# Kernel optimization log

Hardware: AMD Instinct MI355X
Metric: run time of the kernel (lower is better)

The kernel has to match this reference:

```python
import jax, jax.numpy as jnp
import numpy as np
import math

HIDDEN = 2048
N_HEADS = 16
HEAD_DIM = HIDDEN // N_HEADS  # 128
ROPE_THETA = 10000.0


def _rope_cos_sin(seq_len, dim, theta, dtype):
    # Megatron RotaryEmbedding: freqs = pos \outer inv_freq; emb = cat(freqs, freqs)
    inv_freq = 1.0 / (theta ** (jnp.arange(0, dim, 2, dtype=jnp.float32) / dim))
    pos = jnp.arange(seq_len, dtype=jnp.float32)
    freqs = jnp.outer(pos, inv_freq)            # [S, dim/2]
    emb = jnp.concatenate([freqs, freqs], -1)   # [S, dim]
    return jnp.cos(emb).astype(dtype), jnp.sin(emb).astype(dtype)


def _rotate_half(x):
    half = x.shape[-1] // 2
    return jnp.concatenate([-x[..., half:], x[..., :half]], axis=-1)


def setup_inputs() -> dict:
    key = jax.random.key(0)
    k1, k2, k3 = jax.random.split(key, 3)
    B, S = 2, 2048
    hidden_states = jax.random.normal(k1, (B, S, HIDDEN), dtype=jnp.float32)
    # torch Linear weights are [out_features, in_features]
    w_qkv = jax.random.normal(k2, (3 * HIDDEN, HIDDEN), dtype=jnp.float32) * (1.0 / math.sqrt(HIDDEN))
    w_o = jax.random.normal(k3, (HIDDEN, HIDDEN), dtype=jnp.float32) * (1.0 / math.sqrt(HIDDEN))
    return {"hidden_states": hidden_states, "w_qkv": w_qkv, "w_o": w_o}


def reference(hidden_states, w_qkv, w_o):
    B, S, H = hidden_states.shape
    # fused QKV projection: [B,S,H] @ [H, 3H] -> view (.., n_heads, 3, head_dim)
    mixed = jnp.einsum('bsh,oh->bso', hidden_states, w_qkv)
    mixed = mixed.reshape(B, S, N_HEADS, 3, HEAD_DIM)
    q, k, v = mixed[..., 0, :], mixed[..., 1, :], mixed[..., 2, :]  # [B,S,Hn,D]

    # fused split + RoPE (full rotary dim = head_dim)
    cos, sin = _rope_cos_sin(S, HEAD_DIM, ROPE_THETA, hidden_states.dtype)
    cos = cos[None, :, None, :]  # [1,S,1,D]
    sin = sin[None, :, None, :]
    q = q * cos + _rotate_half(q) * sin
    k = k * cos + _rotate_half(k) * sin

    # causal scaled-dot-product attention (flash_attn_func equivalent math)
    scale = 1.0 / math.sqrt(HEAD_DIM)
    scores = jnp.einsum('bqhd,bkhd->bhqk', q, k) * scale  # [B,Hn,S,S]
    causal = jnp.tril(jnp.ones((S, S), dtype=bool))
    scores = jnp.where(causal[None, None], scores, jnp.finfo(scores.dtype).min)
    probs = jax.nn.softmax(scores, axis=-1)
    attn = jnp.einsum('bhqk,bkhd->bqhd', probs, v)  # [B,S,Hn,D]

    attn = attn.reshape(B, S, H)
    out = jnp.einsum('bsh,oh->bso', attn, w_o)
    return out
```

## Files before the change

kernel.cpp:

```cpp
#include <hip/hip_runtime.h>
#include <hip/hip_bf16.h>
#include <cstdint>
#include <cstddef>

#define S_DIM 2048
#define H_DIM 2048
#define NHEAD 16
#define HD_DIM 128
#define O3    6144
#define BS    4096
#define NBH   32

typedef short  s16x4  __attribute__((ext_vector_type(4)));
typedef short  s16x8  __attribute__((ext_vector_type(8)));
typedef __bf16 bf16x8 __attribute__((ext_vector_type(8)));
typedef float  f32x4  __attribute__((ext_vector_type(4)));

__device__ __forceinline__ unsigned short f2bf(float f) {
  unsigned int b = __float_as_uint(f);
  b += 0x7FFFu + ((b >> 16) & 1u);
  return (unsigned short)(b >> 16);
}
__device__ __forceinline__ float bf2f(unsigned short u) {
  return __uint_as_float(((unsigned int)u) << 16);
}
__device__ __forceinline__ bf16x8 load8(const unsigned short* p) {
  s16x8 r = *(const s16x8*)p;
  return __builtin_bit_cast(bf16x8, r);
}
__device__ __forceinline__ f32x4 mfma_bf16(bf16x8 a, bf16x8 b, f32x4 c) {
  return __builtin_amdgcn_mfma_f32_16x16x32_bf16(a, b, c, 0, 0, 0);
}
__device__ __forceinline__ void gload_lds16(const void* g, void* l) {
  __builtin_amdgcn_global_load_lds(
      (__attribute__((address_space(1))) unsigned int*)g,
      (__attribute__((address_space(3))) unsigned int*)l, 16, 0, 0);
}

__global__ void prep_kernel(const float* __restrict__ hid,
                            const float* __restrict__ wqkv,
                            const float* __restrict__ wo,
                            unsigned short* __restrict__ hid_b,
                            unsigned short* __restrict__ wqkv_b,
                            unsigned short* __restrict__ wo_b,
                            float* __restrict__ cosT,
                            float* __restrict__ sinT) {
  const int nA = 2097152, nB = 3145728, nC = 1048576, nD = 131072;
  const int total = nA + nB + nC + nD;
  int stride = gridDim.x * blockDim.x;
  for (int i = blockIdx.x * blockDim.x + threadIdx.x; i < total; i += stride) {
    if (i < nA + nB + nC) {
      const float* src; unsigned short* dst; int j;
      if (i < nA)            { src = hid;  dst = hid_b;  j = i; }
      else if (i < nA + nB)  { src = wqkv; dst = wqkv_b; j = i - nA; }
      else                   { src = wo;   dst = wo_b;   j = i - nA - nB; }
      float4 v = ((const float4*)src)[j];
      ushort4 o;
      o.x = f2bf(v.x); o.y = f2bf(v.y); o.z = f2bf(v.z); o.w = f2bf(v.w);
      ((ushort4*)dst)[j] = o;
    } else {
      int idx = i - nA - nB - nC;
      int s = idx >> 6, d = idx & 63;
      float inv = expf(-((float)d / 64.0f) * 9.210340371976184f);
      float ang = (float)s * inv;
      float sn, cs;
      sincosf(ang, &sn, &cs);
      cosT[idx] = cs;
      sinT[idx] = sn;
    }
  }
}

template <bool OUT_BF16, bool QKV_MAP>
__global__ __launch_bounds__(512, 1)
void gemm3b_kernel(const unsigned short* __restrict__ A,
                   const unsigned short* __restrict__ Bw,
                   void* __restrict__ C, int M, int N, int K) {
  __shared__ __align__(16) unsigned short lA[3][128 * 64];
  __shared__ __align__(16) unsigned short lB[3][256 * 64];
  const int tid  = threadIdx.x;
  const int wave = tid >> 6, lane = tid & 63;
  const int wm = wave >> 2, wn = wave & 3;
  const int lg = lane >> 4, ll = lane & 15;

  const int nbx = gridDim.x;
  const int id  = blockIdx.y * nbx + blockIdx.x;
  int m_tile, n_tile;
  if (QKV_MAP) {
    const int k = id & 7, q = id >> 3;
    const int ng = q >> 5, r = q & 31;
    m_tile = (k >> 1) * 8 + (r & 7);
    n_tile = (k & 1) * 12 + ng * 4 + (r >> 3);
  } else {
    const int nwg = gridDim.x * gridDim.y;
    const int swz = (id & 7) * (nwg >> 3) + (id >> 3);
    m_tile = swz / nbx;
    n_tile = swz % nbx;
  }
  const int m0 = m_tile * 128, n0 = n_tile * 256;

  f32x4 acc[4][4];
#pragma unroll
  for (int i = 0; i < 4; ++i)
#pragma unroll
    for (int j = 0; j < 4; ++j) acc[i][j] = (f32x4){0.f, 0.f, 0.f, 0.f};

  const unsigned short* aP[2];
  const unsigned short* bP[4];
  int aD[2], bD[4];
#pragma unroll
  for (int i = 0; i < 2; ++i) {
    int cb = (i * 8 + wave) * 64 + lane;
    int cs = cb ^ ((cb >> 3) & 7);
    aP[i] = A + (size_t)(m0 + (cs >> 3)) * K + (cs & 7) * 8;
    aD[i] = cb * 8;
  }
#pragma unroll
  for (int i = 0; i < 4; ++i) {
    int cb = (i * 8 + wave) * 64 + lane;
    int cs = cb ^ ((cb >> 3) & 7);
    bP[i] = Bw + (size_t)(n0 + (cs >> 3)) * K + (cs & 7) * 8;
    bD[i] = cb * 8;
  }

  auto STAGE = [&](int buf, int t) {
    const int kt = t << 6;
#pragma unroll
    for (int i = 0; i < 2; ++i) gload_lds16(aP[i] + kt, &lA[buf][aD[i]]);
#pragma unroll
    for (int i = 0; i < 4; ++i) gload_lds16(bP[i] + kt, &lB[buf][bD[i]]);
  };

  const int NT = K >> 6;
  STAGE(0, 0);
  if (NT > 1) {
    STAGE(1, 1);
    asm volatile("s_waitcnt vmcnt(6)" ::: "memory");
  } else {
    asm volatile("s_waitcnt vmcnt(0)" ::: "memory");
  }
  asm volatile("s_barrier" ::: "memory");

  for (int t = 0; t < NT; ++t) {
    const int cur = t % 3;
    const char* lAc = (const char*)&lA[cur][0];
    const char* lBc = (const char*)&lB[cur][0];

    bf16x8 af[4][2], bfr[2][2][2];
#pragma unroll
    for (int fq = 0; fq < 4; ++fq) {
      int r = wm * 64 + fq * 16 + ll;
#pragma unroll
      for (int kk = 0; kk < 2; ++kk) {
        int a = (r * 128 + kk * 64 + lg * 16) ^ ((r & 7) << 4);
        af[fq][kk] = load8((const unsigned short*)(lAc + a));
      }
    }
#pragma unroll
    for (int nh = 0; nh < 2; ++nh)
#pragma unroll
      for (int fq = 0; fq < 2; ++fq) {
        int r = wn * 64 + nh * 32 + fq * 16 + ll;
#pragma unroll
        for (int kk = 0; kk < 2; ++kk) {
          int a = (r * 128 + kk * 64 + lg * 16) ^ ((r & 7) << 4);
          bfr[nh][fq][kk] = load8((const unsigned short*)(lBc + a));
        }
      }

    if (t + 2 < NT) STAGE((t + 2) % 3, t + 2);

    __builtin_amdgcn_s_setprio(1);
#pragma unroll
    for (int nh = 0; nh < 2; ++nh)
#pragma unroll
      for (int fq = 0; fq < 4; ++fq)
#pragma unroll
        for (int gq = 0; gq < 2; ++gq)
#pragma unroll
          for (int kk = 0; kk < 2; ++kk)
            acc[fq][nh * 2 + gq] =
                mfma_bf16(af[fq][kk], bfr[nh][gq][kk], acc[fq][nh * 2 + gq]);
    __builtin_amdgcn_s_setprio(0);

    if (t + 2 < NT)
      asm volatile("s_waitcnt vmcnt(6)" ::: "memory");
    else if (t + 1 < NT)
      asm volatile("s_waitcnt vmcnt(0)" ::: "memory");
    asm volatile("s_barrier" ::: "memory");
  }

#pragma unroll
  for (int fm = 0; fm < 4; ++fm)
#pragma unroll
    for (int fn = 0; fn < 4; ++fn)
#pragma unroll
      for (int j = 0; j < 4; ++j) {
        int r   = m0 + wm * 64 + fm * 16 + lg * 4 + j;
        int col = n0 + wn * 64 + fn * 16 + ll;
        if (OUT_BF16)
          ((unsigned short*)C)[(size_t)r * N + col] = f2bf(acc[fm][fn][j]);
        else
          ((float*)C)[(size_t)r * N + col] = acc[fm][fn][j];
      }
}

__global__ void rope_qk_kernel(const unsigned short* __restrict__ mixed,
                               const float* __restrict__ cosT,
                               const float* __restrict__ sinT,
                               unsigned short* __restrict__ qr,
                               unsigned short* __restrict__ kr) {
  int m = blockIdx.x;
  int s = m & (S_DIM - 1);
  int b = m >> 11;
  const unsigned short* row = mixed + (size_t)m * O3;
  int t = threadIdx.x;
  int h = t >> 4, dg = (t & 15) << 2;
  int base = h * 384;
  s16x4 q0 = *(const s16x4*)(row + base + dg);
  s16x4 q1 = *(const s16x4*)(row + base + 64 + dg);
  s16x4 k0 = *(const s16x4*)(row + base + 128 + dg);
  s16x4 k1 = *(const s16x4*)(row + base + 192 + dg);
  float4 c4 = *(const float4*)(cosT + (s << 6) + dg);
  float4 s4 = *(const float4*)(sinT + (s << 6) + dg);
  size_t ob = ((size_t)(b * NHEAD + h) * S_DIM + s) * HD_DIM;
  s16x4 oq0, oq1, ok0, ok1;
  float cc[4] = {c4.x, c4.y, c4.z, c4.w};
  float ss[4] = {s4.x, s4.y, s4.z, s4.w};
#pragma unroll
  for (int i = 0; i < 4; ++i) {
    float q0f = bf2f((unsigned short)q0[i]), q1f = bf2f((unsigned short)q1[i]);
    float k0f = bf2f((unsigned short)k0[i]), k1f = bf2f((unsigned short)k1[i]);
    oq0[i] = (short)f2bf(q0f * cc[i] - q1f * ss[i]);
    oq1[i] = (short)f2bf(q1f * cc[i] + q0f * ss[i]);
    ok0[i] = (short)f2bf(k0f * cc[i] - k1f * ss[i]);
    ok1[i] = (short)f2bf(k1f * cc[i] + k0f * ss[i]);
  }
  *(s16x4*)(qr + ob + dg)      = oq0;
  *(s16x4*)(qr + ob + 64 + dg) = oq1;
  *(s16x4*)(kr + ob + dg)      = ok0;
  *(s16x4*)(kr + ob + 64 + dg) = ok1;
}

__global__ __launch_bounds__(256)
void vtrans_kernel(const unsigned short* __restrict__ mixed,
                   unsigned short* __restrict__ vt) {
  __shared__ unsigned short t[64 * 65];
  int st = blockIdx.x, dt = blockIdx.y, bh = blockIdx.z;
  int b = bh >> 4, h = bh & 15;
  int s0 = st * 64, d0 = dt * 64;
  int tid = threadIdx.x;
#pragma unroll
  for (int it = 0; it < 2; ++it) {
    int c = it * 256 + tid;
    int sl = c >> 3, dc = c & 7;
    const unsigned short* src =
        mixed + (size_t)(b * S_DIM + s0 + sl) * O3 + h * 384 + 256 + d0 + dc * 8;
    s16x8 v = *(const s16x8*)src;
#pragma unroll
    for (int i = 0; i < 8; ++i) t[(dc * 8 + i) * 65 + sl] = (unsigned short)v[i];
  }
  __syncthreads();
#pragma unroll
  for (int it = 0; it < 2; ++it) {
    int c = it * 256 + tid;
    int dl = c >> 3, sc = c & 7;
    s16x8 v;
#pragma unroll
    for (int i = 0; i < 8; ++i) v[i] = (short)t[dl * 65 + sc * 8 + i];
    *(s16x8*)(vt + ((size_t)bh * HD_DIM + d0 + dl) * S_DIM + s0 + sc * 8) = v;
  }
}

__global__ __launch_bounds__(512, 1)
void attn_kernel(const unsigned short* __restrict__ qr,
                 const unsigned short* __restrict__ kr,
                 const unsigned short* __restrict__ vt,
                 unsigned short* __restrict__ out) {
  __shared__ __align__(16) unsigned short kbuf[2][128 * 128];
  __shared__ __align__(16) unsigned short vbuf[2][128 * 128];
  __shared__ __align__(16) unsigned short plds[8][16 * 72];
  const int p = blockIdx.x, bh = blockIdx.y;
  const int wave = threadIdx.x >> 6, lane = threadIdx.x & 63;
  const int b = bh >> 4, h = bh & 15;
  const int lg = lane >> 4, ll = lane & 15;
  const unsigned short* Qb = qr + (size_t)bh * S_DIM * HD_DIM;
  const unsigned short* Kb = kr + (size_t)bh * S_DIM * HD_DIM;
  const unsigned short* Vb = vt + (size_t)bh * HD_DIM * S_DIM;
  const float kE  = 0.12752792f;
  const float THR = 11.5416f;
  unsigned short* pw = &plds[wave][0];

  for (int seg = 0; seg < 2; ++seg) {
    const int qt = seg ? (15 - p) : p;
    const int qbase = qt * 128 + wave * 16;
    const int ntb = qt + 1;
    const int ntb64 = 2 * qt + 2;

    auto STAGE = [&](int buf, int t) {
      const int k0 = t * 128;
#pragma unroll
      for (int i = 0; i < 4; ++i) {
        int cb = (i * 8 + wave) * 64 + lane;
        int cs = cb ^ ((cb >> 4) & 7);
        gload_lds16(Kb + (size_t)(k0 + (cs >> 4)) * HD_DIM + (cs & 15) * 8,
                    &kbuf[buf][cb * 8]);
      }
#pragma unroll
      for (int i = 0; i < 4; ++i) {
        int cb = (i * 8 + wave) * 64 + lane;
        int cs = cb ^ ((cb >> 4) & 7);
        gload_lds16(Vb + (size_t)(cs >> 4) * S_DIM + k0 + (cs & 15) * 8,
                    &vbuf[buf][cb * 8]);
      }
    };

    bf16x8 aq[4];
#pragma unroll
    for (int kk = 0; kk < 4; ++kk)
      aq[kk] = load8(Qb + (size_t)(qbase + ll) * HD_DIM + kk * 32 + lg * 8);

    float mk[4], lsum[4];
    f32x4 o[8];
#pragma unroll
    for (int j = 0; j < 4; ++j) { mk[j] = -1e30f; lsum[j] = 0.f; }
#pragma unroll
    for (int f = 0; f < 8; ++f) o[f] = (f32x4){0.f, 0.f, 0.f, 0.f};

    STAGE(0, 0);
    __syncthreads();

    for (int t = 0; t < ntb; ++t) {
      const int cur = t & 1;
      if (t + 1 < ntb) STAGE(cur ^ 1, t + 1);
      const char* kb = (const char*)&kbuf[cur][0];
      const char* vb = (const char*)&vbuf[cur][0];

#pragma unroll
      for (int half = 0; half < 2; ++half) {
        const int th = 2 * t + half;
        const int k0h = th * 64;
        const bool maskt = (th >= ntb64 - 2);

        f32x4 s[4];
#pragma unroll
        for (int kf = 0; kf < 4; ++kf) s[kf] = (f32x4){0.f, 0.f, 0.f, 0.f};
        __builtin_amdgcn_s_setprio(1);
#pragma unroll
        for (int kf = 0; kf < 4; ++kf) {
          int r = half * 64 + kf * 16 + ll;
#pragma unroll
          for (int kk = 0; kk < 4; ++kk) {
            int a = (r * 256 + kk * 64 + lg * 16) ^ ((r & 7) << 4);
            s[kf] = mfma_bf16(aq[kk], load8((const unsigned short*)(kb + a)),
                              s[kf]);
          }
        }
        __builtin_amdgcn_s_setprio(0);

        if (maskt) {
#pragma unroll
          for (int kf = 0; kf < 4; ++kf) {
            int kcol = k0h + kf * 16 + ll;
#pragma unroll
            for (int j = 0; j < 4; ++j) {
              int qrow = qbase + lg * 4 + j;
              if (kcol > qrow) s[kf][j] = -1e31f;
            }
          }
        }

        float pmax[4];
        bool ok = true;
#pragma unroll
        for (int j = 0; j < 4; ++j) {
          pmax[j] = fmaxf(fmaxf(s[0][j], s[1][j]), fmaxf(s[2][j], s[3][j]));
          ok = ok && (pmax[j] * kE - mk[j] <= THR);
        }
        if (!__all(ok)) {
#pragma unroll
          for (int j = 0; j < 4; ++j) {
            float rm = pmax[j] * kE;
#pragma unroll
            for (int off = 1; off < 16; off <<= 1)
              rm = fmaxf(rm, __shfl_xor(rm, off, 64));
            rm = fmaxf(rm, mk[j]);
            float corr = exp2f(mk[j] - rm);
            mk[j] = rm;
            lsum[j] *= corr;
#pragma unroll
            for (int f = 0; f < 8; ++f) o[f][j] *= corr;
          }
        }
#pragma unroll
        for (int j = 0; j < 4; ++j) {
          int prow = (lg * 4 + j) * 72;
#pragma unroll
          for (int kf = 0; kf < 4; ++kf) {
            float e = exp2f(fmaf(s[kf][j], kE, -mk[j]));
            lsum[j] += e;
            pw[prow + kf * 16 + ll] = f2bf(e);
          }
        }

        bf16x8 pa0 = load8(&pw[ll * 72 + lg * 8]);
        bf16x8 pa1 = load8(&pw[ll * 72 + 32 + lg * 8]);
        __builtin_amdgcn_s_setprio(1);
#pragma unroll
        for (int f = 0; f < 8; ++f) {
          int rv = f * 16 + ll;
          int a0 = (rv * 256 + half * 128 + lg * 16) ^ ((rv & 7) << 4);
          int a1 = (rv * 256 + half * 128 + 64 + lg * 16) ^ ((rv & 7) << 4);
          o[f] = mfma_bf16(pa0, load8((const unsigned short*)(vb + a0)), o[f]);
          o[f] = mfma_bf16(pa1, load8((const unsigned short*)(vb + a1)), o[f]);
        }
        __builtin_amdgcn_s_setprio(0);
      }

      __syncthreads();
    }

#pragma unroll
    for (int j = 0; j < 4; ++j) {
      float l = lsum[j];
#pragma unroll
      for (int off = 1; off < 16; off <<= 1) l += __shfl_xor(l, off, 64);
      lsum[j] = 1.0f / l;
    }
#pragma unroll
    for (int f = 0; f < 8; ++f)
#pragma unroll
      for (int j = 0; j < 4; ++j) {
        int srow = qbase + lg * 4 + j;
        out[((size_t)(b * S_DIM + srow)) * H_DIM + h * HD_DIM + f * 16 + ll] =
            f2bf(o[f][j] * lsum[j]);
      }
  }
}

extern "C" void kernel_launch(void* const* d_in, const int* in_sizes, int n_in,
                              void* d_out, int out_size, void* d_ws, size_t ws_size,
                              hipStream_t stream) {
  (void)in_sizes; (void)n_in; (void)out_size; (void)ws_size;
  const float* hidden = (const float*)d_in[0];
  const float* wqkv   = (const float*)d_in[1];
  const float* wo     = (const float*)d_in[2];
  char* ws = (char*)d_ws;
  unsigned short* hid_b  = (unsigned short*)(ws);
  unsigned short* wqkv_b = (unsigned short*)(ws + 16777216);
  unsigned short* wo_b   = (unsigned short*)(ws + 41943040);
  unsigned short* mixed  = (unsigned short*)(ws + 50331648);
  unsigned short* q_r    = (unsigned short*)(ws + 100663296);
  unsigned short* k_r    = (unsigned short*)(ws + 117440512);
  unsigned short* v_t    = (unsigned short*)(ws + 134217728);
  unsigned short* attn   = (unsigned short*)(ws + 150994944);
  float* cosT            = (float*)(ws + 167772160);
  float* sinT            = (float*)(ws + 168296448);

  prep_kernel<<<2048, 256, 0, stream>>>(hidden, wqkv, wo, hid_b, wqkv_b, wo_b,
                                        cosT, sinT);

  gemm3b_kernel<true, true><<<dim3(O3 / 256, BS / 128), 512, 0, stream>>>(
      hid_b, wqkv_b, mixed, BS, O3, H_DIM);

  rope_qk_kernel<<<BS, 256, 0, stream>>>(mixed, cosT, sinT, q_r, k_r);
  vtrans_kernel<<<dim3(32, 2, 32), 256, 0, stream>>>(mixed, v_t);

  attn_kernel<<<dim3(8, 32), 512, 0, stream>>>(q_r, k_r, v_t, attn);

  gemm3b_kernel<false, false><<<dim3(H_DIM / 256, BS / 128), 512, 0, stream>>>(
      attn, wo_b, d_out, BS, H_DIM, H_DIM);
}
```

Measured before the change: 264.8 us.

## Fuse RoPE and Q/K head-layout scatter into the QKV GEMM epilogue

After: 254.2 us. -4.0%, faster.

```diff
diff --git a/kernel.cpp b/kernel.cpp
--- a/kernel.cpp
+++ b/kernel.cpp
@@ -71,6 +71,171 @@
   }
 }
 
+__global__ __launch_bounds__(512, 1)
+void gemm_qkv_kernel(const unsigned short* __restrict__ A,
+                     const unsigned short* __restrict__ Bw,
+                     unsigned short* __restrict__ q_r,
+                     unsigned short* __restrict__ k_r,
+                     unsigned short* __restrict__ vc,
+                     const float* __restrict__ cosT,
+                     const float* __restrict__ sinT,
+                     int M, int N, int K) {
+  __shared__ __align__(16) unsigned short lA[3][128 * 64];
+  __shared__ __align__(16) unsigned short lB[3][256 * 64];
+  const int tid  = threadIdx.x;
+  const int wave = tid >> 6, lane = tid & 63;
+  const int wm = wave >> 2, wn = wave & 3;
+  const int lg = lane >> 4, ll = lane & 15;
+
+  const int nbx = gridDim.x;
+  const int id  = blockIdx.y * nbx + blockIdx.x;
+  const int k8 = id & 7, q8 = id >> 3;
+  const int ng = q8 >> 5, r8 = q8 & 31;
+  const int m_tile = (k8 >> 1) * 8 + (r8 & 7);
+  const int n_tile = (k8 & 1) * 12 + ng * 4 + (r8 >> 3);
+  const int m0 = m_tile * 128, n0 = n_tile * 256;
+
+  f32x4 acc[4][4];
+#pragma unroll
+  for (int i = 0; i < 4; ++i)
+#pragma unroll
+    for (int j = 0; j < 4; ++j) acc[i][j] = (f32x4){0.f, 0.f, 0.f, 0.f};
+
+  const unsigned short* aP[2];
+  const unsigned short* bP[4];
+  int aD[2], bD[4];
+#pragma unroll
+  for (int i = 0; i < 2; ++i) {
+    int cb = (i * 8 + wave) * 64 + lane;
+    int cs = cb ^ ((cb >> 3) & 7);
+    aP[i] = A + (size_t)(m0 + (cs >> 3)) * K + (cs & 7) * 8;
+    aD[i] = cb * 8;
+  }
+#pragma unroll
+  for (int i = 0; i < 4; ++i) {
+    int cb = (i * 8 + wave) * 64 + lane;
+    int cs = cb ^ ((cb >> 3) & 7);
+    bP[i] = Bw + (size_t)(n0 + (cs >> 3)) * K + (cs & 7) * 8;
+    bD[i] = cb * 8;
+  }
+
+  auto STAGE = [&](int buf, int t) {
+    const int kt = t << 6;
+#pragma unroll
+    for (int i = 0; i < 2; ++i) gload_lds16(aP[i] + kt, &lA[buf][aD[i]]);
+#pragma unroll
+    for (int i = 0; i < 4; ++i) gload_lds16(bP[i] + kt, &lB[buf][bD[i]]);
+  };
+
+  const int NT = K >> 6;
+  STAGE(0, 0);
+  STAGE(1, 1);
+  asm volatile("s_waitcnt vmcnt(6)" ::: "memory");
+  asm volatile("s_barrier" ::: "memory");
+
+  for (int t = 0; t < NT; ++t) {
+    const int cur = t % 3;
+    const char* lAc = (const char*)&lA[cur][0];
+    const char* lBc = (const char*)&lB[cur][0];
+
+    bf16x8 af[4][2], bfr[2][2][2];
+#pragma unroll
+    for (int fq = 0; fq < 4; ++fq) {
+      int r = wm * 64 + fq * 16 + ll;
+#pragma unroll
+      for (int kk = 0; kk < 2; ++kk) {
+        int a = (r * 128 + kk * 64 + lg * 16) ^ ((r & 7) << 4);
+        af[fq][kk] = load8((const unsigned short*)(lAc + a));
+      }
+    }
+#pragma unroll
+    for (int nh = 0; nh < 2; ++nh)
+#pragma unroll
+      for (int fq = 0; fq < 2; ++fq) {
+        int r = wn * 64 + nh * 32 + fq * 16 + ll;
+#pragma unroll
+        for (int kk = 0; kk < 2; ++kk) {
+          int a = (r * 128 + kk * 64 + lg * 16) ^ ((r & 7) << 4);
+          bfr[nh][fq][kk] = load8((const unsigned short*)(lBc + a));
+        }
+      }
+
+    if (t + 2 < NT) STAGE((t + 2) % 3, t + 2);
+
+    __builtin_amdgcn_s_setprio(1);
+#pragma unroll
+    for (int nh = 0; nh < 2; ++nh)
+#pragma unroll
+      for (int fq = 0; fq < 4; ++fq)
+#pragma unroll
+        for (int gq = 0; gq < 2; ++gq)
+#pragma unroll
+          for (int kk = 0; kk < 2; ++kk)
+            acc[fq][nh * 2 + gq] =
+                mfma_bf16(af[fq][kk], bfr[nh][gq][kk], acc[fq][nh * 2 + gq]);
+    __builtin_amdgcn_s_setprio(0);
+
+    if (t + 2 < NT)
+      asm volatile("s_waitcnt vmcnt(6)" ::: "memory");
+    else if (t + 1 < NT)
+      asm volatile("s_waitcnt vmcnt(0)" ::: "memory");
+    asm volatile("s_barrier" ::: "memory");
+  }
+
+  const int g   = n_tile * 4 + wn;
+  const int sub = g % 6, hh = g / 6;
+  float* slot = (wave < 3) ? (float*)&lA[wave][0]
+                           : (float*)&lB[0][0] + (size_t)(wave - 3) * 4096;
+  const float* pslot = ((wave ^ 1) < 3)
+                           ? (const float*)&lA[wave ^ 1][0]
+                           : (const float*)&lB[0][0] + (size_t)((wave ^ 1) - 3) * 4096;
+#pragma unroll
+  for (int fm = 0; fm < 4; ++fm)
+#pragma unroll
+    for (int fn = 0; fn < 4; ++fn)
+#pragma unroll
+      for (int j = 0; j < 4; ++j)
+        slot[(fm * 16 + fn * 4 + j) * 64 + lane] = acc[fm][fn][j];
+  __syncthreads();
+
+  if (sub < 4) {
+    const bool hi = (sub & 1);
+    unsigned short* dst = (sub < 2) ? q_r : k_r;
+    const int dbase = hi ? 64 : 0;
+#pragma unroll
+    for (int fm = 0; fm < 4; ++fm)
+#pragma unroll
+      for (int fn = 0; fn < 4; ++fn)
+#pragma unroll
+        for (int j = 0; j < 4; ++j) {
+          int r  = m0 + wm * 64 + fm * 16 + lg * 4 + j;
+          int s  = r & (S_DIM - 1), bb = r >> 11;
+          int dp = fn * 16 + ll;
+          float c  = cosT[(s << 6) + dp];
+          float sn = sinT[(s << 6) + dp];
+          float a  = acc[fm][fn][j];
+          float pv = pslot[(fm * 16 + fn * 4 + j) * 64 + lane];
+          float ov = hi ? fmaf(a, c, pv * sn) : fmaf(a, c, -pv * sn);
+          size_t ob = ((size_t)(bb * NHEAD + hh) * S_DIM + s) * HD_DIM
+                      + dbase + dp;
+          dst[ob] = f2bf(ov);
+        }
+  } else {
+    const int dbase = (sub - 4) * 64;
+#pragma unroll
+    for (int fm = 0; fm < 4; ++fm)
+#pragma unroll
+      for (int fn = 0; fn < 4; ++fn)
+#pragma unroll
+        for (int j = 0; j < 4; ++j) {
+          int r  = m0 + wm * 64 + fm * 16 + lg * 4 + j;
+          int dp = fn * 16 + ll;
+          vc[(size_t)r * H_DIM + hh * HD_DIM + dbase + dp] =
+              f2bf(acc[fm][fn][j]);
+        }
+  }
+}
+
 template <bool OUT_BF16, bool QKV_MAP>
 __global__ __launch_bounds__(512, 1)
 void gemm3b_kernel(const unsigned short* __restrict__ A,
@@ -205,45 +370,8 @@
       }
 }
 
-__global__ void rope_qk_kernel(const unsigned short* __restrict__ mixed,
-                               const float* __restrict__ cosT,
-                               const float* __restrict__ sinT,
-                               unsigned short* __restrict__ qr,
-                               unsigned short* __restrict__ kr) {
-  int m = blockIdx.x;
-  int s = m & (S_DIM - 1);
-  int b = m >> 11;
-  const unsigned short* row = mixed + (size_t)m * O3;
-  int t = threadIdx.x;
-  int h = t >> 4, dg = (t & 15) << 2;
-  int base = h * 384;
-  s16x4 q0 = *(const s16x4*)(row + base + dg);
-  s16x4 q1 = *(const s16x4*)(row + base + 64 + dg);
-  s16x4 k0 = *(const s16x4*)(row + base + 128 + dg);
-  s16x4 k1 = *(const s16x4*)(row + base + 192 + dg);
-  float4 c4 = *(const float4*)(cosT + (s << 6) + dg);
-  float4 s4 = *(const float4*)(sinT + (s << 6) + dg);
-  size_t ob = ((size_t)(b * NHEAD + h) * S_DIM + s) * HD_DIM;
-  s16x4 oq0, oq1, ok0, ok1;
-  float cc[4] = {c4.x, c4.y, c4.z, c4.w};
-  float ss[4] = {s4.x, s4.y, s4.z, s4.w};
-#pragma unroll
-  for (int i = 0; i < 4; ++i) {
-    float q0f = bf2f((unsigned short)q0[i]), q1f = bf2f((unsigned short)q1[i]);
-    float k0f = bf2f((unsigned short)k0[i]), k1f = bf2f((unsigned short)k1[i]);
-    oq0[i] = (short)f2bf(q0f * cc[i] - q1f * ss[i]);
-    oq1[i] = (short)f2bf(q1f * cc[i] + q0f * ss[i]);
-    ok0[i] = (short)f2bf(k0f * cc[i] - k1f * ss[i]);
-    ok1[i] = (short)f2bf(k1f * cc[i] + k0f * ss[i]);
-  }
-  *(s16x4*)(qr + ob + dg)      = oq0;
-  *(s16x4*)(qr + ob + 64 + dg) = oq1;
-  *(s16x4*)(kr + ob + dg)      = ok0;
-  *(s16x4*)(kr + ob + 64 + dg) = ok1;
-}
-
 __global__ __launch_bounds__(256)
-void vtrans_kernel(const unsigned short* __restrict__ mixed,
+void vtrans_kernel(const unsigned short* __restrict__ vc,
                    unsigned short* __restrict__ vt) {
   __shared__ unsigned short t[64 * 65];
   int st = blockIdx.x, dt = blockIdx.y, bh = blockIdx.z;
@@ -255,7 +383,7 @@
     int c = it * 256 + tid;
     int sl = c >> 3, dc = c & 7;
     const unsigned short* src =
-        mixed + (size_t)(b * S_DIM + s0 + sl) * O3 + h * 384 + 256 + d0 + dc * 8;
+        vc + (size_t)(b * S_DIM + s0 + sl) * H_DIM + h * HD_DIM + d0 + dc * 8;
     s16x8 v = *(const s16x8*)src;
 #pragma unroll
     for (int i = 0; i < 8; ++i) t[(dc * 8 + i) * 65 + sl] = (unsigned short)v[i];
@@ -449,7 +577,7 @@
   unsigned short* hid_b  = (unsigned short*)(ws);
   unsigned short* wqkv_b = (unsigned short*)(ws + 16777216);
   unsigned short* wo_b   = (unsigned short*)(ws + 41943040);
-  unsigned short* mixed  = (unsigned short*)(ws + 50331648);
+  unsigned short* vc     = (unsigned short*)(ws + 50331648);
   unsigned short* q_r    = (unsigned short*)(ws + 100663296);
   unsigned short* k_r    = (unsigned short*)(ws + 117440512);
   unsigned short* v_t    = (unsigned short*)(ws + 134217728);
@@ -460,11 +588,10 @@
   prep_kernel<<<2048, 256, 0, stream>>>(hidden, wqkv, wo, hid_b, wqkv_b, wo_b,
                                         cosT, sinT);
 
-  gemm3b_kernel<true, true><<<dim3(O3 / 256, BS / 128), 512, 0, stream>>>(
-      hid_b, wqkv_b, mixed, BS, O3, H_DIM);
-
-  rope_qk_kernel<<<BS, 256, 0, stream>>>(mixed, cosT, sinT, q_r, k_r);
-  vtrans_kernel<<<dim3(32, 2, 32), 256, 0, stream>>>(mixed, v_t);
+  gemm_qkv_kernel<<<dim3(O3 / 256, BS / 128), 512, 0, stream>>>(
+      hid_b, wqkv_b, q_r, k_r, vc, cosT, sinT, BS, O3, H_DIM);
+
+  vtrans_kernel<<<dim3(32, 2, 32), 256, 0, stream>>>(vc, v_t);
 
   attn_kernel<<<dim3(8, 32), 512, 0, stream>>>(q_r, k_r, v_t, attn);
 
```
